# Optimization experiments

Hardware: AMD Instinct MI355X
Metric: run time of the kernel (lower is better)

The kernel has to match this reference:

```python
import jax, jax.numpy as jnp
import numpy as np

# Architecture constants (from init_kwargs / ActionConfig)
R = 4          # vae_time_compression_ratio
WS = 2         # windows_size
PAD_T = R * WS # preprocessor left-padding
HID = 512      # action hidden_size
KD_IN = 16     # keyboard_dim_in (movement feature dim)
C_IMG = 3072   # img_hidden_size
KH = 1024      # keyboard_hidden_dim
NH = 16        # heads_num
HD = 64        # keyboard_head_dim
EPS = 1e-6


def setup_inputs() -> dict:
    key = jax.random.key(0)
    ks = jax.random.split(key, 8)
    B, T, Hs, Ws, NF = 1, 3, 44, 80, 81
    S = Hs * Ws

    def w(k, shape, s=0.02):
        return jax.random.normal(k, shape, jnp.float32) * s

    return {
        "x": jax.random.normal(ks[0], (B, T * S, C_IMG), jnp.float32),
        "condition": jax.random.normal(ks[1], (B, NF, KD_IN), jnp.float32),
        "me_w1": w(ks[2], (KD_IN, HID)), "me_b1": jnp.zeros((HID,), jnp.float32),
        "me_w2": w(ks[3], (HID, HID)), "me_b2": jnp.zeros((HID,), jnp.float32),
        "q_w": w(ks[4], (C_IMG, KH)), "q_b": jnp.zeros((KH,), jnp.float32),
        "kv_w": w(ks[5], (HID * WS * R, 2 * KH)), "kv_b": jnp.zeros((2 * KH,), jnp.float32),
        "qn_w": jnp.ones((HD,), jnp.float32), "kn_w": jnp.ones((HD,), jnp.float32),
        "out_w": w(ks[6], (KH, C_IMG)), "out_b": jnp.zeros((C_IMG,), jnp.float32),
        "H": Hs, "W": Ws, "T": T, "num_frame_per_block": T,
    }


def _rmsnorm(x, w):
    return x * jax.lax.rsqrt(jnp.mean(x * x, axis=-1, keepdims=True) + EPS) * w


def _preprocess(condition, me_w1, me_b1, me_w2, me_b2, num_frame_per_block):
    # MovementPreprocessor.forward with is_causal=True
    B, NF, _ = condition.shape
    pad = jnp.broadcast_to(condition[:, :1, :], (B, PAD_T, condition.shape[-1]))
    cp = jnp.concatenate([pad, condition], axis=1)            # [B, PAD_T+NF, KD_IN]
    emb = jax.nn.silu(cp @ me_w1 + me_b1) @ me_w2 + me_b2     # [B, PAD_T+NF, HID]
    n_feats = (NF - 1) // R + 1
    start = R * (n_feats - num_frame_per_block - WS) + PAD_T  # python int (static)
    emb = emb[:, start:, :]
    # vectorized replacement of the python-loop window slicing+stack
    win = jnp.arange(num_frame_per_block)[:, None] * R + jnp.arange(WS * R)[None, :]
    gm = emb[:, win, :]                                       # [B, L, WS*R, HID]
    return gm.reshape(B, num_frame_per_block, WS * R * HID)   # [B, L, 4096]


def reference(x, condition, me_w1, me_b1, me_w2, me_b2, q_w, q_b, kv_w, kv_b,
              qn_w, kn_w, out_w, out_b, H, W, T, num_frame_per_block):
    B = x.shape[0]
    S = H * W
    L = num_frame_per_block

    mf = _preprocess(condition, me_w1, me_b1, me_w2, me_b2, L)  # [B, L, HID*WS*R]

    # q: [B, T*S, C_IMG] -> [B, S, T, h, d]
    q = (x @ q_w + q_b).reshape(B, T, S, NH, HD).transpose(0, 2, 1, 3, 4)

    # k, v: [B, L, h, d] (NOT expanded over S; broadcast inside attention instead)
    kv = (mf @ kv_w + kv_b).reshape(B, L, 2, NH, HD)
    k, v = kv[:, :, 0], kv[:, :, 1]

    q = _rmsnorm(q, qn_w)
    k = _rmsnorm(k, kn_w)

    scale = 1.0 / np.sqrt(HD).astype(np.float32)
    scores = jnp.einsum('bsthd,blhd->bshtl', q, k) * scale      # [B,S,h,T,L]
    attn = jax.nn.softmax(scores, axis=-1)
    o = jnp.einsum('bshtl,blhd->bsthd', attn, v)                # [B,S,T,h,d]

    # '(B S) T H D -> B (T S) (H D)'
    o = o.transpose(0, 2, 1, 3, 4).reshape(B, T * S, NH * HD)
    return x + (o @ out_w + out_b)
```

## Files before the change

### kernel.cpp

```cpp
#include <hip/hip_runtime.h>

#define TOK  10560
#define CIMG 3072
#define KHD  1024

typedef unsigned short ushort_t;
typedef unsigned int u32;
using bf16x8 = __attribute__((ext_vector_type(8))) __bf16;
using f32x4  = __attribute__((ext_vector_type(4))) float;

#define GLD_LDS16(gp, lp) __builtin_amdgcn_global_load_lds( \
    (const __attribute__((address_space(1))) u32*)(gp), \
    (__attribute__((address_space(3))) u32*)(lp), 16, 0, 0)

static __device__ __forceinline__ unsigned short f2bf(float f){
  union { float f; unsigned u; } x; x.f = f;
  unsigned r = x.u + 0x7fffu + ((x.u >> 16) & 1u);
  return (unsigned short)(r >> 16);
}
static __device__ __forceinline__ float wave_sum(float v){
  #pragma unroll
  for (int off = 32; off > 0; off >>= 1) v += __shfl_xor(v, off, 64);
  return v;
}

__global__ __launch_bounds__(256) void k_pre1(const float* __restrict__ cond,
    const float* __restrict__ w1, const float* __restrict__ b1,
    float* __restrict__ h1){
  __shared__ float cs[16][16];
  int t = threadIdx.x;
  if (t < 256) cs[t >> 4][t & 15] = cond[(64 + (t >> 4)) * 16 + (t & 15)];
  __syncthreads();
  #pragma unroll
  for (int i = 0; i < 4; ++i){
    int idx = blockIdx.x * 256 + t + i * 2048;
    int r = idx >> 9, c = idx & 511;
    float s = b1[c];
    #pragma unroll
    for (int j = 0; j < 16; ++j) s += cs[r][j] * w1[j * 512 + c];
    h1[idx] = s / (1.f + __expf(-s));
  }
}

__global__ __launch_bounds__(256) void k_pre2(const float* __restrict__ h1,
    const float* __restrict__ w2, const float* __restrict__ b2,
    float* __restrict__ emb){
  int idx = blockIdx.x * 256 + threadIdx.x;
  int r = idx >> 9, c = idx & 511;
  const float* hp = h1 + r * 512;
  const float* wp = w2 + c;
  float acc = b2[c];
  #pragma unroll 8
  for (int j = 0; j < 512; ++j) acc += hp[j] * wp[(size_t)j * 512];
  emb[idx] = acc;
}

__global__ __launch_bounds__(256) void k_kv(const float* __restrict__ emb,
                                            const float* __restrict__ kvw,
                                            float* __restrict__ part){
  int bl = blockIdx.x;
  int l = bl / 128, rem = bl % 128, nt = rem / 16, kc = rem % 16;
  int n = nt * 256 + threadIdx.x;
  const float* e = emb + 2048 * l + kc * 256;
  const float* w = kvw + (size_t)(kc * 256) * 2048 + n;
  float acc = 0.f;
  for (int r = 0; r < 256; ++r) acc += e[r] * w[(size_t)r * 2048];
  part[kc * 6144 + l * 2048 + n] = acc;
}

__global__ void k_knorm(const float* __restrict__ part, const float* __restrict__ kvb,
                        const float* __restrict__ knw, float* __restrict__ kn,
                        float* __restrict__ vv){
  int wid = threadIdx.x >> 6, lane = threadIdx.x & 63;
  for (int i = 0; i < 12; ++i){
    int g = wid * 12 + i;
    int l = g >> 4, h = g & 15;
    int ik = l * 2048 + h * 64 + lane;
    float kk = kvb[h * 64 + lane];
    float v  = kvb[1024 + h * 64 + lane];
    for (int p = 0; p < 16; ++p){ kk += part[p * 6144 + ik]; v += part[p * 6144 + ik + 1024]; }
    float ss = wave_sum(kk * kk);
    kn[l * 1024 + h * 64 + lane] = kk * rsqrtf(ss * (1.f/64.f) + 1e-6f) * knw[lane];
    vv[l * 1024 + h * 64 + lane] = v;
  }
}

__global__ __launch_bounds__(512) void k_uv(const float* __restrict__ vv,
    const float* __restrict__ ow, float* __restrict__ U){
  int b = blockIdx.x;
  int i = b / 6, cc = b % 6;
  int h = i / 3, l = i % 3;
  int c = cc * 512 + threadIdx.x;
  const float* vp = vv + l * 1024 + h * 64;
  const float* wp = ow + (size_t)(h * 64) * 3072 + c;
  float acc = 0.f;
  #pragma unroll
  for (int d = 0; d < 64; ++d) acc += vp[d] * wp[(size_t)d * 3072];
  U[(size_t)i * 3072 + c] = acc;
}

__global__ __launch_bounds__(256) void k_ubase(const float* __restrict__ U,
    const float* __restrict__ ob, float* __restrict__ base, float* __restrict__ D){
  int c = blockIdx.x * 256 + threadIdx.x;
  float b = ob[c];
  #pragma unroll
  for (int h = 0; h < 16; ++h){
    float u0 = U[(size_t)(h * 3 + 0) * 3072 + c];
    float u1 = U[(size_t)(h * 3 + 1) * 3072 + c];
    float u2 = U[(size_t)(h * 3 + 2) * 3072 + c];
    b += u0;
    D[(size_t)(h * 2 + 0) * 3072 + c] = u1 - u0;
    D[(size_t)(h * 2 + 1) * 3072 + c] = u2 - u0;
  }
  base[c] = b;
}

__global__ __launch_bounds__(256) void k_tconv(const float* __restrict__ src,
                                               ushort_t* __restrict__ dst,
                                               int R, int C){
  __shared__ float tile[32][33];
  int nTr = R >> 5;
  int tr = blockIdx.x % nTr, tc = blockIdx.x / nTr;
  int r0 = tr * 32, c0 = tc * 32, t = threadIdx.x;
  #pragma unroll
  for (int i = 0; i < 4; ++i){
    int idx = t + i * 256; int r = idx >> 5, c = idx & 31;
    tile[r][c] = src[(size_t)(r0 + r) * C + c0 + c];
  }
  __syncthreads();
  #pragma unroll
  for (int i = 0; i < 4; ++i){
    int idx = t + i * 256; int rr = idx >> 5, cc = idx & 31;
    dst[(size_t)(c0 + rr) * R + r0 + cc] = f2bf(tile[cc][rr]);
  }
}

__global__ __launch_bounds__(256) void k_xconv(const float* __restrict__ x,
                                               ushort_t* __restrict__ xb, int n4){
  for (int i = blockIdx.x * 256 + threadIdx.x; i < n4; i += gridDim.x * 256){
    float4 v = ((const float4*)x)[i];
    ushort4 o;
    o.x = f2bf(v.x); o.y = f2bf(v.y); o.z = f2bf(v.z); o.w = f2bf(v.w);
    ((ushort4*)xb)[i] = o;
  }
}

__global__ __launch_bounds__(512, 4) void gemm_fused(
    const ushort_t* __restrict__ A, const ushort_t* __restrict__ Bt,
    const float* __restrict__ bias, const float* __restrict__ kn,
    const float* __restrict__ qnw, float* __restrict__ acoef){
  __shared__ __align__(16) unsigned char lds[81920];
  const int tid = threadIdx.x;
  const int lane = tid & 63, wid = tid >> 6;
  const int wm = wid >> 1, wn = wid & 1;
  const int l15 = lane & 15, kg = lane >> 4;

  int bid = blockIdx.x;
  bid = (bid & 7) * 55 + (bid >> 3);
  const int mt = bid >> 3, nt = bid & 7;
  const int mbase = mt * 192, nbase = nt << 7;

  const int sr  = tid >> 1;
  const int skh = (tid & 1) ^ ((sr >> 2) & 1);
  const ushort_t* gA = A + (size_t)(mbase + sr) * CIMG + skh * 8;
  const int u   = tid - 384;
  const int skb = (u & 1) ^ ((u >> 3) & 1);
  const ushort_t* gB0 = Bt + (size_t)(nbase + (u >> 1)) * CIMG + skb * 8;
  const ushort_t* gB1 = gB0 + (size_t)64 * CIMG;

  auto stage = [&](int t, int b){
    const int gk = t * 64;
    if (wid < 6){
      #pragma unroll
      for (int c = 0; c < 4; ++c)
        GLD_LDS16(gA + gk + c * 16, lds + b * 40960 + c * 6144 + wid * 1024);
    } else {
      #pragma unroll
      for (int c = 0; c < 4; ++c){
        unsigned char* dst = lds + b * 40960 + 24576 + c * 4096 + (wid - 6) * 1024;
        GLD_LDS16(gB0 + gk + c * 16, dst);
        GLD_LDS16(gB1 + gk + c * 16, dst + 2048);
      }
    }
  };

  const int arl = wm * 48 + l15;
  const int brl = wn * 64 + l15;
  const int kh  = ((kg & 1) ^ ((l15 >> 2) & 1)) * 16;
  const unsigned aBase = (unsigned)((kg >> 1) * 6144 + arl * 32 + kh);
  const unsigned bBase = (unsigned)(24576 + (kg >> 1) * 4096 + brl * 32 + kh);

  f32x4 acc[3][4];
  #pragma unroll
  for (int m = 0; m < 3; ++m)
    #pragma unroll
    for (int n = 0; n < 4; ++n) acc[m][n] = {0.f, 0.f, 0.f, 0.f};

  bf16x8 afr[3], bfr[4];

#define PH_READ(base, KSL) { _Pragma("unroll") \
    for (int n = 0; n < 4; ++n) \
      bfr[n] = *(const bf16x8*)((base) + bBase + (KSL)*8192 + n*512); \
    _Pragma("unroll") \
    for (int m = 0; m < 3; ++m) \
      afr[m] = *(const bf16x8*)((base) + aBase + (KSL)*12288 + m*512); }
#define PH_MFMA { __builtin_amdgcn_s_setprio(1); _Pragma("unroll") \
    for (int m = 0; m < 3; ++m){ _Pragma("unroll") \
      for (int n = 0; n < 4; ++n) \
        acc[m][n] = __builtin_amdgcn_mfma_f32_16x16x32_bf16(afr[m], bfr[n], acc[m][n], 0, 0, 0); } \
    __builtin_amdgcn_s_setprio(0); }

  const int T = CIMG / 64;

  stage(0, 0);

  for (int t = 0; t < T; ++t){
    const unsigned char* base = lds + (t & 1) * 40960;
    asm volatile("s_waitcnt vmcnt(0)" ::: "memory");
    __builtin_amdgcn_s_barrier();
    asm volatile("" ::: "memory");
    PH_READ(base, 0);
    if (t + 1 < T) stage(t + 1, (t + 1) & 1);
    PH_MFMA;
    PH_READ(base, 1);
    PH_MFMA;
  }
#undef PH_READ
#undef PH_MFMA

  const int hglob = nt * 2 + wn;
  float qnwv[4], qbv[4], knv0[4], knv1[4], knv2[4];
  #pragma unroll
  for (int n = 0; n < 4; ++n){
    int d = n * 16 + l15;
    qnwv[n] = qnw[d];
    qbv[n]  = bias[nbase + wn * 64 + d];
    knv0[n] = kn[hglob * 64 + d];
    knv1[n] = kn[1024 + hglob * 64 + d];
    knv2[n] = kn[2048 + hglob * 64 + d];
  }
  #pragma unroll
  for (int m = 0; m < 3; ++m){
    #pragma unroll
    for (int j = 0; j < 4; ++j){
      float q[4], ssq = 0.f;
      #pragma unroll
      for (int n = 0; n < 4; ++n){ q[n] = acc[m][n][j] + qbv[n]; ssq += q[n] * q[n]; }
      #pragma unroll
      for (int off = 1; off < 16; off <<= 1) ssq += __shfl_xor(ssq, off, 64);
      float rs = rsqrtf(ssq * (1.f/64.f) + 1e-6f);
      float s0 = 0.f, s1 = 0.f, s2 = 0.f;
      #pragma unroll
      for (int n = 0; n < 4; ++n){
        float qn = q[n] * rs * qnwv[n];
        s0 += qn * knv0[n]; s1 += qn * knv1[n]; s2 += qn * knv2[n];
      }
      #pragma unroll
      for (int off = 1; off < 16; off <<= 1){
        s0 += __shfl_xor(s0, off, 64);
        s1 += __shfl_xor(s1, off, 64);
        s2 += __shfl_xor(s2, off, 64);
      }
      s0 *= 0.125f; s1 *= 0.125f; s2 *= 0.125f;
      float mx = fmaxf(s0, fmaxf(s1, s2));
      float e0 = __expf(s0 - mx), e1 = __expf(s1 - mx), e2 = __expf(s2 - mx);
      float inv = 1.f / (e0 + e1 + e2);
      int grow = mbase + wm * 48 + m * 16 + kg * 4 + j;
      if (l15 == 0){
        float2 a12 = {e1 * inv, e2 * inv};
        *(float2*)(acoef + (size_t)grow * 32 + hglob * 2) = a12;
      }
    }
  }
}

__global__ __launch_bounds__(256) void k_rank32v(const float* __restrict__ x,
    const float* __restrict__ acoef, const float* __restrict__ D,
    const float* __restrict__ base, float* __restrict__ out){
  __shared__ __align__(16) float as[8][32];
  const int tid = threadIdx.x;
  const int rb = blockIdx.x / 3, cc = blockIdx.x % 3;
  const int r0 = rb * 8;
  const int c  = cc * 1024 + tid * 4;

  f32x4 xv[8];
  #pragma unroll
  for (int r = 0; r < 8; ++r)
    xv[r] = *(const f32x4*)(x + (size_t)(r0 + r) * 3072 + c);

  if (tid < 256) ((float*)as)[tid] = acoef[(size_t)r0 * 32 + tid];
  __syncthreads();

  f32x4 accv[8];
  #pragma unroll
  for (int r = 0; r < 8; ++r) accv[r] = {0.f, 0.f, 0.f, 0.f};

  #pragma unroll
  for (int k4 = 0; k4 < 8; ++k4){
    f32x4 d0 = *(const f32x4*)(D + (size_t)(k4 * 4 + 0) * 3072 + c);
    f32x4 d1 = *(const f32x4*)(D + (size_t)(k4 * 4 + 1) * 3072 + c);
    f32x4 d2 = *(const f32x4*)(D + (size_t)(k4 * 4 + 2) * 3072 + c);
    f32x4 d3 = *(const f32x4*)(D + (size_t)(k4 * 4 + 3) * 3072 + c);
    #pragma unroll
    for (int r = 0; r < 8; ++r){
      f32x4 a4 = *(const f32x4*)(&as[r][k4 * 4]);
      accv[r][0] += a4[0]*d0[0] + a4[1]*d1[0] + a4[2]*d2[0] + a4[3]*d3[0];
      accv[r][1] += a4[0]*d0[1] + a4[1]*d1[1] + a4[2]*d2[1] + a4[3]*d3[1];
      accv[r][2] += a4[0]*d0[2] + a4[1]*d1[2] + a4[2]*d2[2] + a4[3]*d3[2];
      accv[r][3] += a4[0]*d0[3] + a4[1]*d1[3] + a4[2]*d2[3] + a4[3]*d3[3];
    }
  }

  f32x4 b4 = *(const f32x4*)(base + c);
  #pragma unroll
  for (int r = 0; r < 8; ++r){
    const size_t o = (size_t)(r0 + r) * 3072 + c;
    f32x4 ov;
    ov[0] = xv[r][0] + b4[0] + accv[r][0];
    ov[1] = xv[r][1] + b4[1] + accv[r][1];
    ov[2] = xv[r][2] + b4[2] + accv[r][2];
    ov[3] = xv[r][3] + b4[3] + accv[r][3];
    *(f32x4*)(out + o) = ov;
  }
}

extern "C" void kernel_launch(void* const* d_in, const int* in_sizes, int n_in,
                              void* d_out, int out_size, void* d_ws, size_t ws_size,
                              hipStream_t stream){
  const float* x    = (const float*)d_in[0];
  const float* cond = (const float*)d_in[1];
  const float* mew1 = (const float*)d_in[2];
  const float* meb1 = (const float*)d_in[3];
  const float* mew2 = (const float*)d_in[4];
  const float* meb2 = (const float*)d_in[5];
  const float* qw   = (const float*)d_in[6];
  const float* qb   = (const float*)d_in[7];
  const float* kvw  = (const float*)d_in[8];
  const float* kvb  = (const float*)d_in[9];
  const float* qnw  = (const float*)d_in[10];
  const float* knw  = (const float*)d_in[11];
  const float* ow   = (const float*)d_in[12];
  const float* ob   = (const float*)d_in[13];

  char* ws = (char*)d_ws;
  float*    emb    = (float*)(ws + 0);
  float*    kvpart = (float*)(ws + 32768);
  float*    kn     = (float*)(ws + 425984);
  float*    vv     = (float*)(ws + 438272);
  ushort_t* qwt    = (ushort_t*)(ws + 450560);
  float*    U      = (float*)(ws + 6742016);
  float*    base   = (float*)(ws + 7331840);
  float*    Dbuf   = (float*)(ws + 7344128);
  float*    acoef  = (float*)(ws + 7737344);
  float*    h1buf  = (float*)(ws + 9089024);

  ushort_t* xb = (ushort_t*)d_out;

  k_pre1<<<8, 256, 0, stream>>>(cond, mew1, meb1, h1buf);
  k_pre2<<<32, 256, 0, stream>>>(h1buf, mew2, meb2, emb);
  k_kv<<<384, 256, 0, stream>>>(emb, kvw, kvpart);
  k_knorm<<<1, 256, 0, stream>>>(kvpart, kvb, knw, kn, vv);
  k_uv<<<288, 512, 0, stream>>>(vv, ow, U);
  k_ubase<<<12, 256, 0, stream>>>(U, ob, base, Dbuf);
  k_tconv<<<3072, 256, 0, stream>>>(qw, qwt, 3072, 1024);
  k_xconv<<<2048, 256, 0, stream>>>(x, xb, (TOK * CIMG) / 4);
  gemm_fused<<<440, 512, 0, stream>>>(xb, qwt, qb, kn, qnw, acoef);
  k_rank32v<<<3960, 256, 0, stream>>>(x, acoef, Dbuf, base, (float*)d_out);
}
```

Measured before the change: 271.0 us.

## Switch GEMM mainloop to 4-stage K=32 LDS ring with depth-3 prefetch

The fused q-projection GEMM mainloop now uses a four-slot ring of K=32 tiles instead of two K=64 buffers. Three stages are in flight, and partial vmcnt waits are tuned per wave role, so global-to-LDS loads have more time to hide behind MFMA work. The LDS layout and XOR swizzle are reworked for 64-byte rows with per-lane precomputed source and destination addresses. In exchange, the loop runs twice as many iterations, so it pays twice as many barriers, with fewer MFMAs between each barrier.

```diff
diff --git a/kernel.cpp b/kernel.cpp
--- a/kernel.cpp
+++ b/kernel.cpp
@@ -160,35 +160,50 @@
   const int mt = bid >> 3, nt = bid & 7;
   const int mbase = mt * 192, nbase = nt << 7;
 
-  const int sr  = tid >> 1;
-  const int skh = (tid & 1) ^ ((sr >> 2) & 1);
-  const ushort_t* gA = A + (size_t)(mbase + sr) * CIMG + skh * 8;
-  const int u   = tid - 384;
-  const int skb = (u & 1) ^ ((u >> 3) & 1);
-  const ushort_t* gB0 = Bt + (size_t)(nbase + (u >> 1)) * CIMG + skb * 8;
-  const ushort_t* gB1 = gB0 + (size_t)64 * CIMG;
-
-  auto stage = [&](int t, int b){
-    const int gk = t * 64;
+  const int skb = ((lane & 3) ^ ((lane >> 4) & 3)) * 8;
+  const int lrow = lane >> 2;
+  const ushort_t *g0, *g1, *g2, *g3;
+  int d0, d1, d2, d3;
+  if (wid < 6){
+    int r0 = (wid * 2 + 0) * 16 + lrow;
+    int r1 = (wid * 2 + 1) * 16 + lrow;
+    g0 = A + (size_t)(mbase + r0) * CIMG + skb;
+    g1 = A + (size_t)(mbase + r1) * CIMG + skb;
+    g2 = g0; g3 = g0;
+    d0 = (wid * 2 + 0) * 1024;
+    d1 = (wid * 2 + 1) * 1024;
+    d2 = d0; d3 = d0;
+  } else {
+    int v = wid - 6;
+    int r0 = (v * 4 + 0) * 16 + lrow, r1 = (v * 4 + 1) * 16 + lrow;
+    int r2 = (v * 4 + 2) * 16 + lrow, r3 = (v * 4 + 3) * 16 + lrow;
+    g0 = Bt + (size_t)(nbase + r0) * CIMG + skb;
+    g1 = Bt + (size_t)(nbase + r1) * CIMG + skb;
+    g2 = Bt + (size_t)(nbase + r2) * CIMG + skb;
+    g3 = Bt + (size_t)(nbase + r3) * CIMG + skb;
+    d0 = 12288 + (v * 4 + 0) * 1024;
+    d1 = 12288 + (v * 4 + 1) * 1024;
+    d2 = 12288 + (v * 4 + 2) * 1024;
+    d3 = 12288 + (v * 4 + 3) * 1024;
+  }
+
+  auto stage = [&](int t){
+    const int gk = t * 32;
+    const int bo = (t & 3) * 20480;
     if (wid < 6){
-      #pragma unroll
-      for (int c = 0; c < 4; ++c)
-        GLD_LDS16(gA + gk + c * 16, lds + b * 40960 + c * 6144 + wid * 1024);
+      GLD_LDS16(g0 + gk, lds + bo + d0);
+      GLD_LDS16(g1 + gk, lds + bo + d1);
     } else {
-      #pragma unroll
-      for (int c = 0; c < 4; ++c){
-        unsigned char* dst = lds + b * 40960 + 24576 + c * 4096 + (wid - 6) * 1024;
-        GLD_LDS16(gB0 + gk + c * 16, dst);
-        GLD_LDS16(gB1 + gk + c * 16, dst + 2048);
-      }
+      GLD_LDS16(g0 + gk, lds + bo + d0);
+      GLD_LDS16(g1 + gk, lds + bo + d1);
+      GLD_LDS16(g2 + gk, lds + bo + d2);
+      GLD_LDS16(g3 + gk, lds + bo + d3);
     }
   };
 
-  const int arl = wm * 48 + l15;
-  const int brl = wn * 64 + l15;
-  const int kh  = ((kg & 1) ^ ((l15 >> 2) & 1)) * 16;
-  const unsigned aBase = (unsigned)((kg >> 1) * 6144 + arl * 32 + kh);
-  const unsigned bBase = (unsigned)(24576 + (kg >> 1) * 4096 + brl * 32 + kh);
+  const int swz = (kg ^ ((l15 >> 2) & 3)) * 16;
+  const unsigned aBase = (unsigned)((wm * 48 + l15) * 64 + swz);
+  const unsigned bBase = (unsigned)(12288 + (wn * 64 + l15) * 64 + swz);
 
   f32x4 acc[3][4];
   #pragma unroll
@@ -198,35 +213,38 @@
 
   bf16x8 afr[3], bfr[4];
 
-#define PH_READ(base, KSL) { _Pragma("unroll") \
-    for (int n = 0; n < 4; ++n) \
-      bfr[n] = *(const bf16x8*)((base) + bBase + (KSL)*8192 + n*512); \
-    _Pragma("unroll") \
-    for (int m = 0; m < 3; ++m) \
-      afr[m] = *(const bf16x8*)((base) + aBase + (KSL)*12288 + m*512); }
-#define PH_MFMA { __builtin_amdgcn_s_setprio(1); _Pragma("unroll") \
-    for (int m = 0; m < 3; ++m){ _Pragma("unroll") \
-      for (int n = 0; n < 4; ++n) \
-        acc[m][n] = __builtin_amdgcn_mfma_f32_16x16x32_bf16(afr[m], bfr[n], acc[m][n], 0, 0, 0); } \
-    __builtin_amdgcn_s_setprio(0); }
-
-  const int T = CIMG / 64;
-
-  stage(0, 0);
+  const int T = CIMG / 32;
+
+  stage(0); stage(1); stage(2);
 
   for (int t = 0; t < T; ++t){
-    const unsigned char* base = lds + (t & 1) * 40960;
-    asm volatile("s_waitcnt vmcnt(0)" ::: "memory");
+    if (t < T - 2){
+      if (wid < 6) asm volatile("s_waitcnt vmcnt(4)" ::: "memory");
+      else         asm volatile("s_waitcnt vmcnt(8)" ::: "memory");
+    } else if (t == T - 2){
+      if (wid < 6) asm volatile("s_waitcnt vmcnt(2)" ::: "memory");
+      else         asm volatile("s_waitcnt vmcnt(4)" ::: "memory");
+    } else {
+      asm volatile("s_waitcnt vmcnt(0)" ::: "memory");
+    }
     __builtin_amdgcn_s_barrier();
     asm volatile("" ::: "memory");
-    PH_READ(base, 0);
-    if (t + 1 < T) stage(t + 1, (t + 1) & 1);
-    PH_MFMA;
-    PH_READ(base, 1);
-    PH_MFMA;
-  }
-#undef PH_READ
-#undef PH_MFMA
+    if (t + 3 < T) stage(t + 3);
+    const unsigned char* base = lds + (t & 3) * 20480;
+    #pragma unroll
+    for (int n = 0; n < 4; ++n)
+      bfr[n] = *(const bf16x8*)(base + bBase + n * 1024);
+    #pragma unroll
+    for (int m = 0; m < 3; ++m)
+      afr[m] = *(const bf16x8*)(base + aBase + m * 1024);
+    __builtin_amdgcn_s_setprio(1);
+    #pragma unroll
+    for (int m = 0; m < 3; ++m)
+      #pragma unroll
+      for (int n = 0; n < 4; ++n)
+        acc[m][n] = __builtin_amdgcn_mfma_f32_16x16x32_bf16(afr[m], bfr[n], acc[m][n], 0, 0, 0);
+    __builtin_amdgcn_s_setprio(0);
+  }
 
   const int hglob = nt * 2 + wn;
   float qnwv[4], qbv[4], knv0[4], knv1[4], knv2[4];
```

New measurement: 260.4 us. 1.04x faster.
